# Optimization experiments

Measured on AMD Instinct MI355X. Metric: run time of the kernel, lower is better.

The kernel has to match this reference:

```python
import jax, jax.numpy as jnp
import numpy as np

B, T, E, H = 1, 4096, 768, 12
DH = E // H


def setup_inputs() -> dict:
    key = jax.random.key(0)
    ks = jax.random.split(key, 10)
    s = 0.02
    inp = {
        "queries": jax.random.normal(ks[0], (B, T, E), jnp.float32),
        "values": jax.random.normal(ks[1], (B, T, E), jnp.float32),
        # causal mask (1 = keep, 0 = masked), matches masked_fill(mask == 0, -1e9)
        "mask": jnp.tril(jnp.ones((T, T), jnp.int32))[None, None, :, :],
        "Wq": jax.random.normal(ks[2], (E, E), jnp.float32) * s,
        "bq": jnp.zeros((E,), jnp.float32),
        "Wk": jax.random.normal(ks[3], (E, E), jnp.float32) * s,
        "bk": jnp.zeros((E,), jnp.float32),
        "Wv": jax.random.normal(ks[4], (E, E), jnp.float32) * s,
        "bv": jnp.zeros((E,), jnp.float32),
        "Wo": jax.random.normal(ks[5], (E, E), jnp.float32) * s,
        "bo": jnp.zeros((E,), jnp.float32),
    }
    return inp


def _split_heads(x):
    # [B,T,E] -> [B,H,T,DH]
    return x.reshape(B, T, H, DH).transpose(0, 2, 1, 3)


def reference(queries, values, mask, Wq, bq, Wk, bk, Wv, bv, Wo, bo):
    # torch nn.Linear: y = x @ W.T + b
    q = _split_heads(queries @ Wq.T + bq)
    k = _split_heads(values @ Wk.T + bk)
    v = _split_heads(values @ Wv.T + bv)
    scale = 1.0 / np.sqrt(DH).astype(np.float32)
    logits = jnp.einsum("bhqd,bhkd->bhqk", q, k) * scale  # [B,H,T,T]
    logits = jnp.where(mask == 0, jnp.float32(-1e9), logits)
    probs = jax.nn.softmax(logits, axis=-1)
    ctx = jnp.einsum("bhqk,bhkd->bhqd", probs, v)  # [B,H,T,DH]
    ctx = ctx.transpose(0, 2, 1, 3).reshape(B, T, E)
    return ctx @ Wo.T + bo
```

## Files before the change

kernel.cpp:

```cpp
#include <hip/hip_runtime.h>
#include <hip/hip_bf16.h>


typedef __hip_bfloat16 bf16;
typedef __attribute__((ext_vector_type(8))) short short8;
typedef __attribute__((ext_vector_type(4))) short short4v;
typedef __attribute__((ext_vector_type(4))) float f32x4;

#define TSEQ 4096
#define NHEAD 12
#define DHEAD 64
#define EMB 768

#if defined(__HIP_DEVICE_COMPILE__)
#define MFMA16(a, b, c) __builtin_amdgcn_mfma_f32_16x16x16bf16_1k(a, b, c, 0, 0, 0)
#else
#define MFMA16(a, b, c) (c)
#endif

typedef const __attribute__((address_space(1))) unsigned int* gptr_t;
typedef __attribute__((address_space(3))) unsigned int* lptr_t;

__device__ __forceinline__ void load_lds16(const void* g, void* l) {
    __builtin_amdgcn_global_load_lds((gptr_t)g, (lptr_t)l, 16, 0, 0);
}

__device__ __forceinline__ float b2f(short s) {
    unsigned u = ((unsigned)(unsigned short)s) << 16;
    float f;
    __builtin_memcpy(&f, &u, 4);
    return f;
}

__device__ __forceinline__ short f2bs(float f) {
    bf16 h = __float2bfloat16(f);
    short s;
    __builtin_memcpy(&s, &h, 2);
    return s;
}

struct CvtJob { const float* src; bf16* dst; int n; };
struct CvtArgs { CvtJob j[6]; };

__global__ __launch_bounds__(256) void cvt_kernel(CvtArgs a) {
    const CvtJob jb = a.j[blockIdx.y];
    const int i = (blockIdx.x * 256 + threadIdx.x) * 8;
    if (i >= jb.n) return;
    const float4 x0 = *(const float4*)(jb.src + i);
    const float4 x1 = *(const float4*)(jb.src + i + 4);
    bf16 tmp[8];
    tmp[0] = __float2bfloat16(x0.x); tmp[1] = __float2bfloat16(x0.y);
    tmp[2] = __float2bfloat16(x0.z); tmp[3] = __float2bfloat16(x0.w);
    tmp[4] = __float2bfloat16(x1.x); tmp[5] = __float2bfloat16(x1.y);
    tmp[6] = __float2bfloat16(x1.z); tmp[7] = __float2bfloat16(x1.w);
    *(short8*)(jb.dst + i) = *(const short8*)tmp;
}

template<int NF>
__device__ __forceinline__ void gemm_t(
    const bf16* __restrict__ A, const bf16* __restrict__ W,
    const float* __restrict__ bias,
    bf16* __restrict__ outb, float* __restrict__ outf,
    const int mode, const float scale, const int m0, const int n0,
    bf16* sA, bf16* sB)
{
    const int tid  = threadIdx.x;
    const int lane = tid & 63;
    const int wave = tid >> 6;
    const int wr = wave >> 1, wc = wave & 1;
    const int lg = lane >> 4, lr = lane & 15;

    f32x4 acc[4][NF];
#pragma unroll
    for (int m = 0; m < 4; ++m)
#pragma unroll
        for (int n = 0; n < NF; ++n)
            acc[m][n] = (f32x4){0.f, 0.f, 0.f, 0.f};

    for (int k0 = 0; k0 < EMB; k0 += 64) {
        if (k0) __syncthreads();
#pragma unroll
        for (int is = 0; is < 4; ++is) {
            const int chunk = is * 256 + tid;
            const int row = chunk >> 3;
            const int csw = (chunk & 7) ^ (row & 7);
            load_lds16(A + (size_t)(m0 + row) * EMB + k0 + csw * 8,
                       sA + is * 2048 + wave * 512);
        }
#pragma unroll
        for (int is = 0; is < NF; ++is) {
            const int chunk = is * 256 + tid;
            const int row = chunk >> 3;
            const int csw = (chunk & 7) ^ (row & 7);
            load_lds16(W + (size_t)(n0 + row) * EMB + k0 + csw * 8,
                       sB + is * 2048 + wave * 512);
        }
        __syncthreads();

        short8 af[4][2], bfv[NF][2];
#pragma unroll
        for (int m = 0; m < 4; ++m)
#pragma unroll
            for (int kk = 0; kk < 2; ++kk) {
                const int row = wr * 64 + m * 16 + lr;
                const int cc = (kk * 4 + lg) ^ (row & 7);
                af[m][kk] = *(const short8*)(sA + row * 64 + cc * 8);
            }
#pragma unroll
        for (int n = 0; n < NF; ++n)
#pragma unroll
            for (int kk = 0; kk < 2; ++kk) {
                const int row = wc * (NF * 16) + n * 16 + lr;
                const int cc = (kk * 4 + lg) ^ (row & 7);
                bfv[n][kk] = *(const short8*)(sB + row * 64 + cc * 8);
            }
#pragma unroll
        for (int kk = 0; kk < 2; ++kk)
#pragma unroll
            for (int m = 0; m < 4; ++m)
#pragma unroll
                for (int n = 0; n < NF; ++n)
                    acc[m][n] = __builtin_amdgcn_mfma_f32_16x16x32_bf16(
                        af[m][kk], bfv[n][kk], acc[m][n], 0, 0, 0);
    }

#pragma unroll
    for (int n = 0; n < NF; ++n) {
        const int o = n0 + wc * (NF * 16) + n * 16 + lr;
        const float bv = bias[o];
#pragma unroll
        for (int m = 0; m < 4; ++m) {
            const int tbase = m0 + wr * 64 + m * 16 + lg * 4;
#pragma unroll
            for (int r = 0; r < 4; ++r) {
                const float v = (acc[m][n][r] + bv) * scale;
                const int t = tbase + r;
                if (mode == 0)
                    outb[(size_t)(o >> 6) * TSEQ * DHEAD + (size_t)t * DHEAD + (o & 63)] =
                        __float2bfloat16(v);
                else if (mode == 1)
                    outb[(size_t)(o >> 6) * DHEAD * TSEQ + (size_t)(o & 63) * TSEQ + t] =
                        __float2bfloat16(v);
                else
                    outf[(size_t)t * EMB + o] = v;
            }
        }
    }
}

struct QkvArgs {
    const bf16 *xq, *xv, *Wq, *Wk, *Wv;
    const float *bq, *bk, *bv;
    bf16 *qo, *ko, *vto;
};

__global__ __launch_bounds__(256) void qkv_gemm(QkvArgs a) {
    __shared__ __attribute__((aligned(16))) bf16 sA[128 * 64];
    __shared__ __attribute__((aligned(16))) bf16 sB[128 * 64];
    const int z = blockIdx.z;
    const bf16* A = (z == 0) ? a.xq : a.xv;
    const bf16* W = (z == 0) ? a.Wq : (z == 1 ? a.Wk : a.Wv);
    const float* b = (z == 0) ? a.bq : (z == 1 ? a.bk : a.bv);
    bf16* o = (z == 0) ? a.qo : (z == 1 ? a.ko : a.vto);
    const int mode = (z == 2) ? 1 : 0;
    const float scale = (z == 0) ? 0.18033688011112042f : 1.0f;
    gemm_t<4>(A, W, b, o, nullptr, mode, scale, blockIdx.x * 128, blockIdx.y * 128, sA, sB);
}

__global__ __launch_bounds__(256) void out_gemm(
    const bf16* __restrict__ ctx, const bf16* __restrict__ Wo,
    const float* __restrict__ bo, float* __restrict__ out)
{
    __shared__ __attribute__((aligned(16))) bf16 sA[128 * 64];
    __shared__ __attribute__((aligned(16))) bf16 sB[64 * 64];
    gemm_t<2>(ctx, Wo, bo, nullptr, out, 2, 1.0f, blockIdx.x * 128, blockIdx.y * 64, sA, sB);
}

struct AttnState {
    f32x4 O[4];
    float m, l;
};

__device__ __forceinline__ void stage_tile(
    const bf16* __restrict__ Kh, const bf16* __restrict__ Vh,
    bf16* sK, bf16* sV, const int kv0, const int tid)
{
    const int wave = tid >> 6;
#pragma unroll
    for (int is = 0; is < 2; ++is) {
        const int chunk = is * 256 + tid;
        const int row = chunk >> 3;
        const int csw = (chunk & 7) ^ (row & 7);
        load_lds16(Kh + (size_t)(kv0 + row) * DHEAD + csw * 8,
                   sK + is * 2048 + wave * 512);
        load_lds16(Vh + (size_t)row * TSEQ + kv0 + csw * 8,
                   sV + is * 2048 + wave * 512);
    }
}

template<int BUF>
__device__ __forceinline__ void attn_tile(
    const bf16* kp0, const bf16* kp1,
    const bf16* vp0, const bf16* vp1, const bf16* vp2, const bf16* vp3,
    const short8 (&qf)[2], AttnState& st,
    const int kv0, const int qw, const int lane)
{
    const int lg = lane >> 4, lr = lane & 15;
    if (kv0 > qw + 15) return;

    f32x4 s[4];
    short8 kf[4][2];
#pragma unroll
    for (int n = 0; n < 4; ++n) {
        kf[n][0] = *(const short8*)(kp0 + BUF * 4096 + n * 1024);
        kf[n][1] = *(const short8*)(kp1 + BUF * 4096 + n * 1024);
    }
#pragma unroll
    for (int n = 0; n < 4; ++n) s[n] = (f32x4){0.f, 0.f, 0.f, 0.f};
#pragma unroll
    for (int kk = 0; kk < 2; ++kk)
#pragma unroll
        for (int n = 0; n < 4; ++n)
            s[n] = __builtin_amdgcn_mfma_f32_16x16x32_bf16(
                kf[n][kk], qf[kk], s[n], 0, 0, 0);

    if (kv0 + 63 > qw) {
        const int qi = qw + lr;
#pragma unroll
        for (int n = 0; n < 4; ++n) {
            const int kb = kv0 + n * 16 + lg * 4;
#pragma unroll
            for (int r = 0; r < 4; ++r)
                if (kb + r > qi) s[n][r] = -3.0e38f;
        }
    }

    const float a0 = fmaxf(fmaxf(s[0][0], s[0][1]), fmaxf(s[0][2], s[0][3]));
    const float a1 = fmaxf(fmaxf(s[1][0], s[1][1]), fmaxf(s[1][2], s[1][3]));
    const float a2 = fmaxf(fmaxf(s[2][0], s[2][1]), fmaxf(s[2][2], s[2][3]));
    const float a3 = fmaxf(fmaxf(s[3][0], s[3][1]), fmaxf(s[3][2], s[3][3]));
    float mx = fmaxf(fmaxf(a0, a1), fmaxf(a2, a3));
    mx = fmaxf(mx, __shfl_xor(mx, 16));
    mx = fmaxf(mx, __shfl_xor(mx, 32));

    const float mn = fmaxf(st.m, mx);
    const float al = __builtin_amdgcn_exp2f(st.m - mn);
    st.m = mn;

    float rsn[4];
    short4v pq[4];
#pragma unroll
    for (int n = 0; n < 4; ++n) {
        const float p0 = __builtin_amdgcn_exp2f(s[n][0] - mn);
        const float p1 = __builtin_amdgcn_exp2f(s[n][1] - mn);
        const float p2 = __builtin_amdgcn_exp2f(s[n][2] - mn);
        const float p3 = __builtin_amdgcn_exp2f(s[n][3] - mn);
        rsn[n] = (p0 + p1) + (p2 + p3);
        pq[n][0] = f2bs(p0); pq[n][1] = f2bs(p1);
        pq[n][2] = f2bs(p2); pq[n][3] = f2bs(p3);
    }
    float rs = (rsn[0] + rsn[1]) + (rsn[2] + rsn[3]);
    rs += __shfl_xor(rs, 16);
    rs += __shfl_xor(rs, 32);
    st.l = st.l * al + rs;

#pragma unroll
    for (int nd = 0; nd < 4; ++nd)
#pragma unroll
        for (int r = 0; r < 4; ++r)
            st.O[nd][r] *= al;

#pragma unroll
    for (int nd = 0; nd < 4; ++nd) {
        f32x4 o = st.O[nd];
        o = MFMA16(*(const short4v*)(vp0 + BUF * 4096 + nd * 1024), pq[0], o);
        o = MFMA16(*(const short4v*)(vp1 + BUF * 4096 + nd * 1024), pq[1], o);
        o = MFMA16(*(const short4v*)(vp2 + BUF * 4096 + nd * 1024), pq[2], o);
        o = MFMA16(*(const short4v*)(vp3 + BUF * 4096 + nd * 1024), pq[3], o);
        st.O[nd] = o;
    }
}

__global__ __launch_bounds__(256, 4) void attn_kernel(
    const bf16* __restrict__ Q, const bf16* __restrict__ K,
    const bf16* __restrict__ VT, bf16* __restrict__ Opart,
    float* __restrict__ ml, const int nch_max, const int U)
{
    __shared__ __attribute__((aligned(16))) bf16 sK[2][64 * 64];
    __shared__ __attribute__((aligned(16))) bf16 sV[2][64 * 64];

    const int tid  = threadIdx.x;
    const int lane = tid & 63;
    const int wave = tid >> 6;
    const int lg = lane >> 4, lr = lane & 15;

    const int bid = blockIdx.x;
    const int h = bid % 12;
    int rem = (U - 1) - (bid / 12);
    int g = 0;
    while (g < 7) {
        const int cap = (g + 1 < nch_max) ? g + 1 : nch_max;
        const int gu = 8 * cap;
        if (rem < gu) break;
        rem -= gu;
        ++g;
    }
    const int d = (g + 1 < nch_max) ? g + 1 : nch_max;
    const int bx = 8 * g + rem / d;
    const int c = rem % d;

    const int q0 = bx * 64;
    const int qw = q0 + wave * 16;
    const int S = bx + 1;
    const int t0 = (c * S) / d;
    const int t1 = ((c + 1) * S) / d;

    const bf16* Qh = Q  + (size_t)h * TSEQ * DHEAD;
    const bf16* Kh = K  + (size_t)h * TSEQ * DHEAD;
    const bf16* Vh = VT + (size_t)h * DHEAD * TSEQ;

    short8 qf[2];
#pragma unroll
    for (int kk = 0; kk < 2; ++kk)
        qf[kk] = *(const short8*)(Qh + (size_t)(qw + lr) * DHEAD + kk * 32 + lg * 8);

    const int kb0 = lr * 64 + ((lg ^ (lr & 7)) * 8);
    const bf16* kp0 = &sK[0][0] + kb0;
    const bf16* kp1 = &sK[0][0] + (kb0 ^ 32);
    const int vx = ((lg >> 1) ^ (lr & 7)) * 8;
    const int vb = lr * 64 + (lg & 1) * 4;
    const bf16* vp0 = &sV[0][0] + vb + (0 ^ vx);
    const bf16* vp1 = &sV[0][0] + vb + (16 ^ vx);
    const bf16* vp2 = &sV[0][0] + vb + (32 ^ vx);
    const bf16* vp3 = &sV[0][0] + vb + (48 ^ vx);

    AttnState st;
#pragma unroll
    for (int nd = 0; nd < 4; ++nd) st.O[nd] = (f32x4){0.f, 0.f, 0.f, 0.f};
    st.m = -3.0e38f; st.l = 0.f;

    stage_tile(Kh, Vh, &sK[0][0], &sV[0][0], t0 * 64, tid);
    __syncthreads();

    int it = t0;
    while (it < t1) {
        if (it + 1 < t1) stage_tile(Kh, Vh, &sK[1][0], &sV[1][0], (it + 1) * 64, tid);
        attn_tile<0>(kp0, kp1, vp0, vp1, vp2, vp3, qf, st, it * 64, qw, lane);
        __syncthreads();
        ++it;
        if (it >= t1) break;
        if (it + 1 < t1) stage_tile(Kh, Vh, &sK[0][0], &sV[0][0], (it + 1) * 64, tid);
        attn_tile<1>(kp0, kp1, vp0, vp1, vp2, vp3, qf, st, it * 64, qw, lane);
        __syncthreads();
        ++it;
    }

    const int u = (h * 64 + bx) * nch_max + c;
    bf16* op = Opart + (size_t)u * 4096;
    float* mlp = ml + (size_t)u * 128;
    const int q = wave * 16 + lr;
#pragma unroll
    for (int nd = 0; nd < 4; ++nd) {
        short4v ov;
        ov[0] = f2bs(st.O[nd][0]); ov[1] = f2bs(st.O[nd][1]);
        ov[2] = f2bs(st.O[nd][2]); ov[3] = f2bs(st.O[nd][3]);
        *(short4v*)(op + q * 64 + nd * 16 + lg * 4) = ov;
    }
    if (lg == 0) {
        mlp[q] = st.m;
        mlp[64 + q] = st.l;
    }
}

__global__ __launch_bounds__(256) void combine_kernel(
    const bf16* __restrict__ Opart, const float* __restrict__ ml,
    bf16* __restrict__ ctx, const int nch_max)
{
    const int h  = blockIdx.y;
    const int bx = blockIdx.x;
    const int tid = threadIdx.x;
    const int row = tid >> 2;
    const int dp  = (tid & 3) * 16;
    const int ub = (h * 64 + bx) * nch_max;
    const int g = bx >> 3;
    const int nchb = (nch_max > 1) ? ((g + 1 < nch_max) ? g + 1 : nch_max) : 1;

    float M = -3.0e38f;
    for (int c = 0; c < nchb; ++c)
        M = fmaxf(M, ml[(size_t)(ub + c) * 128 + row]);

    float L = 0.f;
    float acc[16];
#pragma unroll
    for (int i = 0; i < 16; ++i) acc[i] = 0.f;
    for (int c = 0; c < nchb; ++c) {
        const float mc = ml[(size_t)(ub + c) * 128 + row];
        const float lc = ml[(size_t)(ub + c) * 128 + 64 + row];
        const float w = __builtin_amdgcn_exp2f(mc - M);
        L += lc * w;
        const bf16* op = Opart + ((size_t)(ub + c) * 64 + row) * 64 + dp;
        const short8 v0 = *(const short8*)op;
        const short8 v1 = *(const short8*)(op + 8);
#pragma unroll
        for (int i = 0; i < 8; ++i) acc[i] += w * b2f(v0[i]);
#pragma unroll
        for (int i = 0; i < 8; ++i) acc[8 + i] += w * b2f(v1[i]);
    }
    const float invL = 1.0f / L;

    bf16 outv[16];
#pragma unroll
    for (int i = 0; i < 16; ++i) outv[i] = __float2bfloat16(acc[i] * invL);
    const int t = bx * 64 + row;
    bf16* dst = ctx + (size_t)t * EMB + h * DHEAD + dp;
    *(short8*)dst = *(const short8*)outv;
    *(short8*)(dst + 8) = *(const short8*)(outv + 8);
}

extern "C" void kernel_launch(void* const* d_in, const int* in_sizes, int n_in,
                              void* d_out, int out_size, void* d_ws, size_t ws_size,
                              hipStream_t stream) {
    const float* queries = (const float*)d_in[0];
    const float* values  = (const float*)d_in[1];
    const float* Wq = (const float*)d_in[3];
    const float* bq = (const float*)d_in[4];
    const float* Wk = (const float*)d_in[5];
    const float* bk = (const float*)d_in[6];
    const float* Wv = (const float*)d_in[7];
    const float* bv = (const float*)d_in[8];
    const float* Wo = (const float*)d_in[9];
    const float* bo = (const float*)d_in[10];
    float* out = (float*)d_out;

    const size_t NTE = (size_t)TSEQ * EMB;
    const size_t WSZ = (size_t)EMB * EMB;
    bf16* ws  = (bf16*)d_ws;
    bf16* qb  = ws;
    bf16* vb  = qb + NTE;
    bf16* wqb = vb + NTE;
    bf16* wkb = wqb + WSZ;
    bf16* wvb = wkb + WSZ;
    bf16* wob = wvb + WSZ;
    bf16* qh  = wob + WSZ;
    bf16* kh  = qh + NTE;
    bf16* vth = kh + NTE;
    bf16* ctx = qb;

    const size_t fixed_elems = 5 * NTE + 4 * WSZ;
    int nch = 8;
    for (;;) {
        const size_t units = (size_t)NHEAD * (TSEQ / 64) * nch;
        const size_t need = fixed_elems * 2 + units * 4096 * 2 + units * 128 * 4;
        if (ws_size >= need || nch == 1) break;
        nch = (nch == 8) ? 4 : 1;
    }
    const size_t units = (size_t)NHEAD * (TSEQ / 64) * nch;
    bf16* opart = ws + fixed_elems;
    float* ml = (float*)(opart + units * 4096);

    int U = 0;
    for (int g = 0; g < 8; ++g) U += 8 * ((g + 1 < nch) ? g + 1 : nch);

    CvtArgs ca;
    ca.j[0] = {queries, qb,  (int)NTE};
    ca.j[1] = {values,  vb,  (int)NTE};
    ca.j[2] = {Wq,      wqb, (int)WSZ};
    ca.j[3] = {Wk,      wkb, (int)WSZ};
    ca.j[4] = {Wv,      wvb, (int)WSZ};
    ca.j[5] = {Wo,      wob, (int)WSZ};
    cvt_kernel<<<dim3((NTE + 2047) / 2048, 6), 256, 0, stream>>>(ca);

    QkvArgs a{qb, vb, wqb, wkb, wvb, bq, bk, bv, qh, kh, vth};
    qkv_gemm<<<dim3(TSEQ / 128, EMB / 128, 3), 256, 0, stream>>>(a);
    attn_kernel<<<dim3(12 * U), 256, 0, stream>>>(qh, kh, vth, opart, ml, nch, U);
    combine_kernel<<<dim3(TSEQ / 64, NHEAD), 256, 0, stream>>>(opart, ml, ctx, nch);
    out_gemm<<<dim3(TSEQ / 128, EMB / 64), 256, 0, stream>>>(ctx, wob, bo, out);
}
```

Before: 115.0 us.

## Triple-buffer K/V tiles with prefetch two ahead and partial vmcnt waits

```diff
diff --git a/kernel.cpp b/kernel.cpp
--- a/kernel.cpp
+++ b/kernel.cpp
@@ -281,13 +281,35 @@
     }
 }
 
+template<int B>
+__device__ __forceinline__ void attn_step(
+    const bf16* __restrict__ Kh, const bf16* __restrict__ Vh,
+    bf16* sK, bf16* sV,
+    const bf16* kp0, const bf16* kp1,
+    const bf16* vp0, const bf16* vp1, const bf16* vp2, const bf16* vp3,
+    const short8 (&qf)[2], AttnState& st,
+    const int it, const int t1, const int qw, const int lane, const int tid)
+{
+    asm volatile("s_waitcnt lgkmcnt(0)" ::: "memory");
+    if (it + 1 < t1) asm volatile("s_waitcnt vmcnt(4)" ::: "memory");
+    else             asm volatile("s_waitcnt vmcnt(0)" ::: "memory");
+    __builtin_amdgcn_sched_barrier(0);
+    __builtin_amdgcn_s_barrier();
+    __builtin_amdgcn_sched_barrier(0);
+    if (it + 2 < t1) {
+        constexpr int NB = (B + 2) % 3;
+        stage_tile(Kh, Vh, sK + NB * 4096, sV + NB * 4096, (it + 2) * 64, tid);
+    }
+    attn_tile<B>(kp0, kp1, vp0, vp1, vp2, vp3, qf, st, it * 64, qw, lane);
+}
+
 __global__ __launch_bounds__(256, 4) void attn_kernel(
     const bf16* __restrict__ Q, const bf16* __restrict__ K,
     const bf16* __restrict__ VT, bf16* __restrict__ Opart,
     float* __restrict__ ml, const int nch_max, const int U)
 {
-    __shared__ __attribute__((aligned(16))) bf16 sK[2][64 * 64];
-    __shared__ __attribute__((aligned(16))) bf16 sV[2][64 * 64];
+    __shared__ __attribute__((aligned(16))) bf16 sK[3 * 4096];
+    __shared__ __attribute__((aligned(16))) bf16 sV[3 * 4096];
 
     const int tid  = threadIdx.x;
     const int lane = tid & 63;
@@ -325,33 +347,31 @@
         qf[kk] = *(const short8*)(Qh + (size_t)(qw + lr) * DHEAD + kk * 32 + lg * 8);
 
     const int kb0 = lr * 64 + ((lg ^ (lr & 7)) * 8);
-    const bf16* kp0 = &sK[0][0] + kb0;
-    const bf16* kp1 = &sK[0][0] + (kb0 ^ 32);
+    const bf16* kp0 = sK + kb0;
+    const bf16* kp1 = sK + (kb0 ^ 32);
     const int vx = ((lg >> 1) ^ (lr & 7)) * 8;
     const int vb = lr * 64 + (lg & 1) * 4;
-    const bf16* vp0 = &sV[0][0] + vb + (0 ^ vx);
-    const bf16* vp1 = &sV[0][0] + vb + (16 ^ vx);
-    const bf16* vp2 = &sV[0][0] + vb + (32 ^ vx);
-    const bf16* vp3 = &sV[0][0] + vb + (48 ^ vx);
+    const bf16* vp0 = sV + vb + (0 ^ vx);
+    const bf16* vp1 = sV + vb + (16 ^ vx);
+    const bf16* vp2 = sV + vb + (32 ^ vx);
+    const bf16* vp3 = sV + vb + (48 ^ vx);
 
     AttnState st;
 #pragma unroll
     for (int nd = 0; nd < 4; ++nd) st.O[nd] = (f32x4){0.f, 0.f, 0.f, 0.f};
     st.m = -3.0e38f; st.l = 0.f;
 
-    stage_tile(Kh, Vh, &sK[0][0], &sV[0][0], t0 * 64, tid);
-    __syncthreads();
+    stage_tile(Kh, Vh, sK, sV, t0 * 64, tid);
+    if (t0 + 1 < t1)
+        stage_tile(Kh, Vh, sK + 4096, sV + 4096, (t0 + 1) * 64, tid);
 
     int it = t0;
     while (it < t1) {
-        if (it + 1 < t1) stage_tile(Kh, Vh, &sK[1][0], &sV[1][0], (it + 1) * 64, tid);
-        attn_tile<0>(kp0, kp1, vp0, vp1, vp2, vp3, qf, st, it * 64, qw, lane);
-        __syncthreads();
-        ++it;
-        if (it >= t1) break;
-        if (it + 1 < t1) stage_tile(Kh, Vh, &sK[0][0], &sV[0][0], (it + 1) * 64, tid);
-        attn_tile<1>(kp0, kp1, vp0, vp1, vp2, vp3, qf, st, it * 64, qw, lane);
-        __syncthreads();
+        attn_step<0>(Kh, Vh, sK, sV, kp0, kp1, vp0, vp1, vp2, vp3, qf, st, it, t1, qw, lane, tid);
+        ++it; if (it >= t1) break;
+        attn_step<1>(Kh, Vh, sK, sV, kp0, kp1, vp0, vp1, vp2, vp3, qf, st, it, t1, qw, lane, tid);
+        ++it; if (it >= t1) break;
+        attn_step<2>(Kh, Vh, sK, sV, kp0, kp1, vp0, vp1, vp2, vp3, qf, st, it, t1, qw, lane, tid);
         ++it;
     }
 
```

Measured after the change: 122.5 us. 1.07x slower.

## Load K/V fragments directly from global memory instead of LDS double buffering

Applied to the files above, without the earlier changes.

```diff
diff --git a/kernel.cpp b/kernel.cpp
--- a/kernel.cpp
+++ b/kernel.cpp
@@ -181,114 +181,11 @@
     float m, l;
 };
 
-__device__ __forceinline__ void stage_tile(
-    const bf16* __restrict__ Kh, const bf16* __restrict__ Vh,
-    bf16* sK, bf16* sV, const int kv0, const int tid)
-{
-    const int wave = tid >> 6;
-#pragma unroll
-    for (int is = 0; is < 2; ++is) {
-        const int chunk = is * 256 + tid;
-        const int row = chunk >> 3;
-        const int csw = (chunk & 7) ^ (row & 7);
-        load_lds16(Kh + (size_t)(kv0 + row) * DHEAD + csw * 8,
-                   sK + is * 2048 + wave * 512);
-        load_lds16(Vh + (size_t)row * TSEQ + kv0 + csw * 8,
-                   sV + is * 2048 + wave * 512);
-    }
-}
-
-template<int BUF>
-__device__ __forceinline__ void attn_tile(
-    const bf16* kp0, const bf16* kp1,
-    const bf16* vp0, const bf16* vp1, const bf16* vp2, const bf16* vp3,
-    const short8 (&qf)[2], AttnState& st,
-    const int kv0, const int qw, const int lane)
-{
-    const int lg = lane >> 4, lr = lane & 15;
-    if (kv0 > qw + 15) return;
-
-    f32x4 s[4];
-    short8 kf[4][2];
-#pragma unroll
-    for (int n = 0; n < 4; ++n) {
-        kf[n][0] = *(const short8*)(kp0 + BUF * 4096 + n * 1024);
-        kf[n][1] = *(const short8*)(kp1 + BUF * 4096 + n * 1024);
-    }
-#pragma unroll
-    for (int n = 0; n < 4; ++n) s[n] = (f32x4){0.f, 0.f, 0.f, 0.f};
-#pragma unroll
-    for (int kk = 0; kk < 2; ++kk)
-#pragma unroll
-        for (int n = 0; n < 4; ++n)
-            s[n] = __builtin_amdgcn_mfma_f32_16x16x32_bf16(
-                kf[n][kk], qf[kk], s[n], 0, 0, 0);
-
-    if (kv0 + 63 > qw) {
-        const int qi = qw + lr;
-#pragma unroll
-        for (int n = 0; n < 4; ++n) {
-            const int kb = kv0 + n * 16 + lg * 4;
-#pragma unroll
-            for (int r = 0; r < 4; ++r)
-                if (kb + r > qi) s[n][r] = -3.0e38f;
-        }
-    }
-
-    const float a0 = fmaxf(fmaxf(s[0][0], s[0][1]), fmaxf(s[0][2], s[0][3]));
-    const float a1 = fmaxf(fmaxf(s[1][0], s[1][1]), fmaxf(s[1][2], s[1][3]));
-    const float a2 = fmaxf(fmaxf(s[2][0], s[2][1]), fmaxf(s[2][2], s[2][3]));
-    const float a3 = fmaxf(fmaxf(s[3][0], s[3][1]), fmaxf(s[3][2], s[3][3]));
-    float mx = fmaxf(fmaxf(a0, a1), fmaxf(a2, a3));
-    mx = fmaxf(mx, __shfl_xor(mx, 16));
-    mx = fmaxf(mx, __shfl_xor(mx, 32));
-
-    const float mn = fmaxf(st.m, mx);
-    const float al = __builtin_amdgcn_exp2f(st.m - mn);
-    st.m = mn;
-
-    float rsn[4];
-    short4v pq[4];
-#pragma unroll
-    for (int n = 0; n < 4; ++n) {
-        const float p0 = __builtin_amdgcn_exp2f(s[n][0] - mn);
-        const float p1 = __builtin_amdgcn_exp2f(s[n][1] - mn);
-        const float p2 = __builtin_amdgcn_exp2f(s[n][2] - mn);
-        const float p3 = __builtin_amdgcn_exp2f(s[n][3] - mn);
-        rsn[n] = (p0 + p1) + (p2 + p3);
-        pq[n][0] = f2bs(p0); pq[n][1] = f2bs(p1);
-        pq[n][2] = f2bs(p2); pq[n][3] = f2bs(p3);
-    }
-    float rs = (rsn[0] + rsn[1]) + (rsn[2] + rsn[3]);
-    rs += __shfl_xor(rs, 16);
-    rs += __shfl_xor(rs, 32);
-    st.l = st.l * al + rs;
-
-#pragma unroll
-    for (int nd = 0; nd < 4; ++nd)
-#pragma unroll
-        for (int r = 0; r < 4; ++r)
-            st.O[nd][r] *= al;
-
-#pragma unroll
-    for (int nd = 0; nd < 4; ++nd) {
-        f32x4 o = st.O[nd];
-        o = MFMA16(*(const short4v*)(vp0 + BUF * 4096 + nd * 1024), pq[0], o);
-        o = MFMA16(*(const short4v*)(vp1 + BUF * 4096 + nd * 1024), pq[1], o);
-        o = MFMA16(*(const short4v*)(vp2 + BUF * 4096 + nd * 1024), pq[2], o);
-        o = MFMA16(*(const short4v*)(vp3 + BUF * 4096 + nd * 1024), pq[3], o);
-        st.O[nd] = o;
-    }
-}
-
 __global__ __launch_bounds__(256, 4) void attn_kernel(
     const bf16* __restrict__ Q, const bf16* __restrict__ K,
     const bf16* __restrict__ VT, bf16* __restrict__ Opart,
     float* __restrict__ ml, const int nch_max, const int U)
 {
-    __shared__ __attribute__((aligned(16))) bf16 sK[2][64 * 64];
-    __shared__ __attribute__((aligned(16))) bf16 sV[2][64 * 64];
-
     const int tid  = threadIdx.x;
     const int lane = tid & 63;
     const int wave = tid >> 6;
@@ -324,35 +221,97 @@
     for (int kk = 0; kk < 2; ++kk)
         qf[kk] = *(const short8*)(Qh + (size_t)(qw + lr) * DHEAD + kk * 32 + lg * 8);
 
-    const int kb0 = lr * 64 + ((lg ^ (lr & 7)) * 8);
-    const bf16* kp0 = &sK[0][0] + kb0;
-    const bf16* kp1 = &sK[0][0] + (kb0 ^ 32);
-    const int vx = ((lg >> 1) ^ (lr & 7)) * 8;
-    const int vb = lr * 64 + (lg & 1) * 4;
-    const bf16* vp0 = &sV[0][0] + vb + (0 ^ vx);
-    const bf16* vp1 = &sV[0][0] + vb + (16 ^ vx);
-    const bf16* vp2 = &sV[0][0] + vb + (32 ^ vx);
-    const bf16* vp3 = &sV[0][0] + vb + (48 ^ vx);
+    const bf16* krow[4];
+#pragma unroll
+    for (int n = 0; n < 4; ++n)
+        krow[n] = Kh + (size_t)(n * 16 + lr) * DHEAD + lg * 8;
+    const bf16* vrow[4];
+#pragma unroll
+    for (int nd = 0; nd < 4; ++nd)
+        vrow[nd] = Vh + (size_t)(nd * 16 + lr) * TSEQ + lg * 4;
 
     AttnState st;
 #pragma unroll
     for (int nd = 0; nd < 4; ++nd) st.O[nd] = (f32x4){0.f, 0.f, 0.f, 0.f};
     st.m = -3.0e38f; st.l = 0.f;
 
-    stage_tile(Kh, Vh, &sK[0][0], &sV[0][0], t0 * 64, tid);
-    __syncthreads();
-
-    int it = t0;
-    while (it < t1) {
-        if (it + 1 < t1) stage_tile(Kh, Vh, &sK[1][0], &sV[1][0], (it + 1) * 64, tid);
-        attn_tile<0>(kp0, kp1, vp0, vp1, vp2, vp3, qf, st, it * 64, qw, lane);
-        __syncthreads();
-        ++it;
-        if (it >= t1) break;
-        if (it + 1 < t1) stage_tile(Kh, Vh, &sK[0][0], &sV[0][0], (it + 1) * 64, tid);
-        attn_tile<1>(kp0, kp1, vp0, vp1, vp2, vp3, qf, st, it * 64, qw, lane);
-        __syncthreads();
-        ++it;
+    for (int it = t0; it < t1; ++it) {
+        const int kv0 = it * 64;
+        if (kv0 > qw + 15) break;
+
+        short8 kf[4][2];
+#pragma unroll
+        for (int n = 0; n < 4; ++n) {
+            const bf16* kr = krow[n] + (size_t)kv0 * DHEAD;
+            kf[n][0] = *(const short8*)(kr);
+            kf[n][1] = *(const short8*)(kr + 32);
+        }
+        f32x4 s[4];
+#pragma unroll
+        for (int n = 0; n < 4; ++n) s[n] = (f32x4){0.f, 0.f, 0.f, 0.f};
+#pragma unroll
+        for (int kk = 0; kk < 2; ++kk)
+#pragma unroll
+            for (int n = 0; n < 4; ++n)
+                s[n] = __builtin_amdgcn_mfma_f32_16x16x32_bf16(
+                    kf[n][kk], qf[kk], s[n], 0, 0, 0);
+
+        if (kv0 + 63 > qw) {
+            const int qi = qw + lr;
+#pragma unroll
+            for (int n = 0; n < 4; ++n) {
+                const int kb = kv0 + n * 16 + lg * 4;
+#pragma unroll
+                for (int r = 0; r < 4; ++r)
+                    if (kb + r > qi) s[n][r] = -3.0e38f;
+            }
+        }
+
+        const float a0 = fmaxf(fmaxf(s[0][0], s[0][1]), fmaxf(s[0][2], s[0][3]));
+        const float a1 = fmaxf(fmaxf(s[1][0], s[1][1]), fmaxf(s[1][2], s[1][3]));
+        const float a2 = fmaxf(fmaxf(s[2][0], s[2][1]), fmaxf(s[2][2], s[2][3]));
+        const float a3 = fmaxf(fmaxf(s[3][0], s[3][1]), fmaxf(s[3][2], s[3][3]));
+        float mx = fmaxf(fmaxf(a0, a1), fmaxf(a2, a3));
+        mx = fmaxf(mx, __shfl_xor(mx, 16));
+        mx = fmaxf(mx, __shfl_xor(mx, 32));
+
+        const float mn = fmaxf(st.m, mx);
+        const float al = __builtin_amdgcn_exp2f(st.m - mn);
+        st.m = mn;
+
+        float rsn[4];
+        short4v pq[4];
+#pragma unroll
+        for (int n = 0; n < 4; ++n) {
+            const float p0 = __builtin_amdgcn_exp2f(s[n][0] - mn);
+            const float p1 = __builtin_amdgcn_exp2f(s[n][1] - mn);
+            const float p2 = __builtin_amdgcn_exp2f(s[n][2] - mn);
+            const float p3 = __builtin_amdgcn_exp2f(s[n][3] - mn);
+            rsn[n] = (p0 + p1) + (p2 + p3);
+            pq[n][0] = f2bs(p0); pq[n][1] = f2bs(p1);
+            pq[n][2] = f2bs(p2); pq[n][3] = f2bs(p3);
+        }
+        float rs = (rsn[0] + rsn[1]) + (rsn[2] + rsn[3]);
+        rs += __shfl_xor(rs, 16);
+        rs += __shfl_xor(rs, 32);
+        st.l = st.l * al + rs;
+
+#pragma unroll
+        for (int nd = 0; nd < 4; ++nd)
+#pragma unroll
+            for (int r = 0; r < 4; ++r)
+                st.O[nd][r] *= al;
+
+#pragma unroll
+        for (int nd = 0; nd < 4; ++nd) {
+            const bf16* vr = vrow[nd] + kv0;
+            f32x4 o = st.O[nd];
+            o = MFMA16(*(const short4v*)(vr),      pq[0], o);
+            o = MFMA16(*(const short4v*)(vr + 16), pq[1], o);
+            o = MFMA16(*(const short4v*)(vr + 32), pq[2], o);
+            o = MFMA16(*(const short4v*)(vr + 48), pq[3], o);
+            st.O[nd] = o;
+        }
     }
 
     const int u = (h * 64 + bx) * nch_max + c;
```

Measured after the change: 340.6 us. 2.96x slower.
